# Kernel optimization log

Measured on AMD Instinct MI355X. Metric: run time of the kernel, lower is better.

The kernel has to match this reference:

```python
import jax, jax.numpy as jnp
import numpy as np

L, H, C, DH, FF = 6, 8, 512, 64, 2048
B, T, S = 64, 128, 128
EPS = 1e-5


def setup_inputs() -> dict:
    key = jax.random.key(0)
    ks = jax.random.split(key, 20)
    sc = 0.02
    def w(k, shape):
        return jax.random.normal(k, shape, dtype=jnp.float32) * sc
    inp = {
        "x": jax.random.normal(ks[0], (B, T, C), dtype=jnp.float32),
        "encoder_output": jax.random.normal(ks[1], (B, S, C), dtype=jnp.float32),
        # per-head self-attention projections, stacked over layers and heads
        "sa_wq": w(ks[2], (L, H, C, DH)), "sa_bq": w(ks[3], (L, H, DH)),
        "sa_wk": w(ks[4], (L, H, C, DH)), "sa_bk": w(ks[5], (L, H, DH)),
        "sa_wv": w(ks[6], (L, H, C, DH)), "sa_bv": w(ks[7], (L, H, DH)),
        # per-head cross-attention projections
        "ca_wq": w(ks[8], (L, H, C, DH)), "ca_bq": w(ks[9], (L, H, DH)),
        "ca_wk": w(ks[10], (L, H, C, DH)), "ca_bk": w(ks[11], (L, H, DH)),
        "ca_wv": w(ks[12], (L, H, C, DH)), "ca_bv": w(ks[13], (L, H, DH)),
        # feed-forward
        "ff_w1": w(ks[14], (L, C, FF)), "ff_b1": w(ks[15], (L, FF)),
        "ff_w2": w(ks[16], (L, FF, C)), "ff_b2": w(ks[17], (L, C)),
    }
    return inp


def _layer_norm_2d(x):
    # F.layer_norm(x, (T, C)): normalize jointly over last two dims, no affine
    mu = jnp.mean(x, axis=(1, 2), keepdims=True)
    var = jnp.var(x, axis=(1, 2), keepdims=True)
    return (x - mu) * jax.lax.rsqrt(var + EPS)


def _mha(qx, kvx, wq, bq, wk, bk, wv, bv):
    # wq/wk/wv: [H, C, DH]; per-head projections, vectorized over heads.
    q = jnp.einsum("btc,hcd->bhtd", qx, wq) + bq[:, None, :]
    k = jnp.einsum("bsc,hcd->bhsd", kvx, wk) + bk[:, None, :]
    v = jnp.einsum("bsc,hcd->bhsd", kvx, wv) + bv[:, None, :]
    scores = jax.nn.softmax(jnp.einsum("bhtd,bhsd->bhts", q, k) * (DH ** -0.5), axis=-1)
    out = jnp.einsum("bhts,bhsd->bhtd", scores, v)
    b, h, t, d = out.shape  # concat heads along feature dim
    return out.transpose(0, 2, 1, 3).reshape(b, t, h * d)


def reference(x, encoder_output, sa_wq, sa_bq, sa_wk, sa_bk, sa_wv, sa_bv,
              ca_wq, ca_bq, ca_wk, ca_bk, ca_wv, ca_bv,
              ff_w1, ff_b1, ff_w2, ff_b2):
    for l in range(L):
        # masked MHA (note: original code never applies the causal mask)
        x = x + _mha(x, x, sa_wq[l], sa_bq[l], sa_wk[l], sa_bk[l], sa_wv[l], sa_bv[l])
        x = _layer_norm_2d(x)
        # cross attention: q from decoder, k/v from encoder output
        x = x + _mha(x, encoder_output, ca_wq[l], ca_bq[l], ca_wk[l], ca_bk[l], ca_wv[l], ca_bv[l])
        x = _layer_norm_2d(x)
        # feed-forward
        h = jax.nn.relu(jnp.einsum("btc,cf->btf", x, ff_w1[l]) + ff_b1[l])
        x = x + (jnp.einsum("btf,fc->btc", h, ff_w2[l]) + ff_b2[l])
        x = _layer_norm_2d(x)
    return x
```

## Files before the change

kernel.cpp:

```cpp
#include <hip/hip_runtime.h>
#include <hip/hip_bf16.h>


typedef __bf16 bf16;
typedef bf16 bf16x8 __attribute__((ext_vector_type(8)));
typedef float f32x4 __attribute__((ext_vector_type(4)));

#define MFMA16(a, b, c) __builtin_amdgcn_mfma_f32_16x16x32_bf16(a, b, c, 0, 0, 0)

#define GLL16(gsrc, ldst)                                                          \
    __builtin_amdgcn_global_load_lds(                                              \
        (const __attribute__((address_space(1))) void*)(gsrc),                     \
        (__attribute__((address_space(3))) void*)(ldst), 16, 0, 0)

static constexpr int L_ = 6, C_ = 512, FF_ = 2048;
static constexpr int B_ = 64, T_ = 128;
static constexpr int M_ = B_ * T_;
static constexpr float LNINV = 1.f / 65536.f;
static constexpr float EPS_ = 1e-5f;

__global__ __launch_bounds__(256) void zero_all(
    float* __restrict__ csA, float* __restrict__ csQ, float* __restrict__ csF,
    float* __restrict__ part)
{
    const int i = blockIdx.x * 256 + threadIdx.x;
    if (i < 6 * 1536) csA[i] = 0.f;
    if (i < 6 * 512)  csQ[i] = 0.f;
    if (i < 6 * 2048) csF[i] = 0.f;
    if (i < 18 * 64 * 2) part[i] = 0.f;
}

__global__ __launch_bounds__(256) void init_x(
    const float* __restrict__ xin, float* __restrict__ y, bf16* __restrict__ yb)
{
    const size_t i = ((size_t)blockIdx.x * 256 + threadIdx.x) * 8;
    float4 f0 = *(const float4*)(xin + i);
    float4 f1 = *(const float4*)(xin + i + 4);
    *(float4*)(y + i) = f0;
    *(float4*)(y + i + 4) = f1;
    bf16x8 v = {(bf16)f0.x, (bf16)f0.y, (bf16)f0.z, (bf16)f0.w,
                (bf16)f1.x, (bf16)f1.y, (bf16)f1.z, (bf16)f1.w};
    *(bf16x8*)(yb + i) = v;
}

__global__ __launch_bounds__(256) void to_bf16(
    const float* __restrict__ in, bf16* __restrict__ out)
{
    const size_t i = ((size_t)blockIdx.x * 256 + threadIdx.x) * 8;
    float4 f0 = *(const float4*)(in + i);
    float4 f1 = *(const float4*)(in + i + 4);
    bf16x8 v = {(bf16)f0.x, (bf16)f0.y, (bf16)f0.z, (bf16)f0.w,
                (bf16)f1.x, (bf16)f1.y, (bf16)f1.z, (bf16)f1.w};
    *(bf16x8*)(out + i) = v;
}

__global__ __launch_bounds__(256) void ff_repack(
    const float* __restrict__ ff_w1, const float* __restrict__ ff_w2,
    bf16* __restrict__ W1, bf16* __restrict__ W2)
{
    __shared__ alignas(16) float t[64][68];
    const int z = blockIdx.z;
    const float* src;
    bf16* dst;
    int R, C, r0, c0;
    if (z < 6) {
        src = ff_w1 + (size_t)z * 512 * 2048;
        dst = W1 + (size_t)z * 2048 * 512;
        R = 512; C = 2048;
        r0 = blockIdx.y * 64;
        c0 = blockIdx.x * 64;
    } else {
        src = ff_w2 + (size_t)(z - 6) * 2048 * 512;
        dst = W2 + (size_t)(z - 6) * 512 * 2048;
        R = 2048; C = 512;
        r0 = (blockIdx.y * 4 + (blockIdx.x >> 3)) * 64;
        c0 = (blockIdx.x & 7) * 64;
    }
    const int tr = threadIdx.x >> 4;
    const int tc = (threadIdx.x & 15) * 4;
#pragma unroll
    for (int ro = 0; ro < 64; ro += 16)
        *(float4*)&t[tr + ro][tc] = *(const float4*)(src + (size_t)(r0 + tr + ro) * C + c0 + tc);
    __syncthreads();
    const int wc = (threadIdx.x & 7) * 8;
#pragma unroll
    for (int po = 0; po < 2; ++po) {
        const int oc = (threadIdx.x >> 3) + po * 32;
        bf16x8 v;
#pragma unroll
        for (int j = 0; j < 8; ++j) v[j] = (bf16)t[wc + j][oc];
        *(bf16x8*)(dst + (size_t)(c0 + oc) * R + r0 + wc) = v;
    }
}

__global__ __launch_bounds__(256) void head_repack(
    const float* __restrict__ sa_wq, const float* __restrict__ sa_wk,
    const float* __restrict__ sa_wv, const float* __restrict__ ca_wq,
    const float* __restrict__ ca_wk, const float* __restrict__ ca_wv,
    bf16* __restrict__ Wsa, bf16* __restrict__ Wcaq, bf16* __restrict__ Wcakv)
{
    __shared__ alignas(16) float t[64][68];
    const int z = blockIdx.z;
    const int type = z / 48, rem = z % 48, l = rem >> 3, h = rem & 7;
    const float* srcs[6] = {sa_wq, sa_wk, sa_wv, ca_wq, ca_wk, ca_wv};
    const float* s = srcs[type] + (size_t)(l * 8 + h) * 512 * 64;
    bf16* d;
    if (type < 3)       d = Wsa   + ((size_t)l * 1536 + type * 512 + h * 64) * 512;
    else if (type == 3) d = Wcaq  + ((size_t)l * 512 + h * 64) * 512;
    else                d = Wcakv + ((size_t)l * 1024 + (type - 4) * 512 + h * 64) * 512;
    const int r0 = blockIdx.y * 64;
    const int tr = threadIdx.x >> 4;
    const int tc = (threadIdx.x & 15) * 4;
#pragma unroll
    for (int ro = 0; ro < 64; ro += 16)
        *(float4*)&t[tr + ro][tc] = *(const float4*)(s + (size_t)(r0 + tr + ro) * 64 + tc);
    __syncthreads();
    const int wc = (threadIdx.x & 7) * 8;
#pragma unroll
    for (int po = 0; po < 2; ++po) {
        const int oc = (threadIdx.x >> 3) + po * 32;
        bf16x8 v;
#pragma unroll
        for (int j = 0; j < 8; ++j) v[j] = (bf16)t[wc + j][oc];
        *(bf16x8*)(d + (size_t)oc * 512 + r0 + wc) = v;
    }
}

__global__ __launch_bounds__(256) void colsum_all(
    const float* __restrict__ sa_wq, const float* __restrict__ sa_wk,
    const float* __restrict__ sa_wv, const float* __restrict__ ca_wq,
    const float* __restrict__ ff_w1,
    float* __restrict__ csA, float* __restrict__ csQ, float* __restrict__ csF)
{
    const int t = blockIdx.x * 256 + threadIdx.x;
    const int l = t >> 12, u = t & 4095;
    const int r0 = blockIdx.y * 64;
    const float* base;
    int stride;
    float* out;
    if (u < 1536) {
        const int p = u >> 9, h = (u >> 6) & 7, d = u & 63;
        const float* w = (p == 0) ? sa_wq : (p == 1) ? sa_wk : sa_wv;
        base = w + (size_t)(l * 8 + h) * 512 * 64 + d;
        stride = 64;
        out = &csA[l * 1536 + u];
    } else if (u < 2048) {
        const int v = u - 1536, h = v >> 6, d = v & 63;
        base = ca_wq + (size_t)(l * 8 + h) * 512 * 64 + d;
        stride = 64;
        out = &csQ[l * 512 + v];
    } else {
        const int f = u - 2048;
        base = ff_w1 + (size_t)l * 512 * 2048 + f;
        stride = 2048;
        out = &csF[l * 2048 + f];
    }
    const float* p = base + (size_t)r0 * stride;
    float s0 = 0.f, s1 = 0.f, s2 = 0.f, s3 = 0.f;
#pragma unroll 4
    for (int c = 0; c < 64; c += 4) {
        s0 += p[0];
        s1 += p[(size_t)stride];
        s2 += p[(size_t)2 * stride];
        s3 += p[(size_t)3 * stride];
        p += (size_t)4 * stride;
    }
    atomicAdd(out, (s0 + s1) + (s2 + s3));
}

template <int MODE, int BN>
__global__ __launch_bounds__(256, 4) void gemm_bt(
    const bf16* __restrict__ A, const bf16* __restrict__ BT,
    const float* __restrict__ b0, const float* __restrict__ b1,
    const float* __restrict__ b2, const float* __restrict__ cs,
    float2* __restrict__ part, int slotPrev, int slotNew,
    bf16* __restrict__ o0, bf16* __restrict__ o1, bf16* __restrict__ o2,
    float* __restrict__ y, bf16* __restrict__ ybf, int N, int K)
{
    constexpr int MI = 4;
    constexpr int NI = BN / 32;
    constexpr int BGLL = BN / 64;
    constexpr int VG = 2 + BGLL;
    __shared__ alignas(16) bf16 as[2][128][32];
    __shared__ alignas(16) bf16 bs[2][BN][32];
    const int tid = threadIdx.x, wave = tid >> 6, lane = tid & 63;

    const int gx = gridDim.x;
    int wgid = blockIdx.y * gx + blockIdx.x;
    {
        const int nwg = gx * gridDim.y;
        const int q = nwg >> 3, r = nwg & 7;
        const int xcd = wgid & 7, idx = wgid >> 3;
        wgid = (xcd < r ? xcd * (q + 1) : r * (q + 1) + (xcd - r) * q) + idx;
    }
    const int m0 = (wgid / gx) * 128, n0 = (wgid % gx) * BN;

    const int wr = (wave >> 1) * 64;
    const int wc = (wave & 1) * (BN / 2);
    const int fr = lane & 15, fq = lane >> 4;
    const int xr = fr & 3;

    float mu = 0.f, rstd = 1.f;
    if (slotPrev >= 0) {
        float2 p = part[slotPrev * 64 + (m0 >> 7)];
        mu = p.x * LNINV;
        rstd = rsqrtf(p.y * LNINV - mu * mu + EPS_);
    }

    const int rlane = lane >> 2;
    const int scol = ((lane & 3) ^ (rlane & 3)) * 8;
    const bf16* pa = A + (size_t)(m0 + wave * 32 + rlane) * K + scol;
    const bf16* pb = BT + (size_t)(n0 + wave * (BGLL * 16) + rlane) * K + scol;

    auto stage = [&](int buf, int k0) {
#pragma unroll
        for (int i = 0; i < 2; ++i)
            GLL16(pa + k0 + (size_t)(16 * i) * K, &as[buf][wave * 32 + 16 * i][0]);
#pragma unroll
        for (int i = 0; i < BGLL; ++i)
            GLL16(pb + k0 + (size_t)(16 * i) * K, &bs[buf][wave * (BGLL * 16) + 16 * i][0]);
    };

    f32x4 acc[MI][NI] = {};
    bf16x8 af[MI], bfv[NI];
    auto frags = [&](int buf) {
#pragma unroll
        for (int mi = 0; mi < MI; ++mi)
            af[mi] = *(const bf16x8*)&as[buf][wr + mi * 16 + fr][(fq ^ xr) << 3];
#pragma unroll
        for (int ni = 0; ni < NI; ++ni)
            bfv[ni] = *(const bf16x8*)&bs[buf][wc + ni * 16 + fr][(fq ^ xr) << 3];
    };
    auto cluster = [&]() {
#pragma unroll
        for (int mi = 0; mi < MI; ++mi)
#pragma unroll
            for (int ni = 0; ni < NI; ++ni)
                acc[mi][ni] = MFMA16(af[mi], bfv[ni], acc[mi][ni]);
    };

    const int nt = K >> 5;
    stage(0, 0);
    stage(1, 32);

    int cur = 0;
    for (int t = 0; t < nt - 1; ++t) {
        asm volatile("s_waitcnt vmcnt(%0)\n\ts_barrier" :: "n"(VG) : "memory");
        frags(cur);
        asm volatile("s_waitcnt lgkmcnt(0)\n\ts_barrier" ::: "memory");
        if (t + 2 < nt) stage(cur, (t + 2) << 5);
        cluster();
        cur ^= 1;
    }
    asm volatile("s_waitcnt vmcnt(0)\n\ts_barrier" ::: "memory");
    frags(cur);
    cluster();

    float s = 0.f, ss = 0.f;
    const float murs = mu * rstd;
#pragma unroll
    for (int mi = 0; mi < MI; ++mi) {
#pragma unroll
        for (int ni = 0; ni < NI; ++ni) {
            const int n = n0 + wc + ni * 16 + fr;
#pragma unroll
            for (int reg = 0; reg < 4; ++reg) {
                const int r = m0 + wr + mi * 16 + fq * 4 + reg;
                float val = acc[mi][ni][reg];
                if constexpr (MODE == 0) {
                    const int p = n >> 9, hd = n & 511, d = n & 63, hh = (n >> 6) & 7;
                    const int bb = r >> 7, tt = r & 127;
                    const float* bias = (p == 0) ? b0 : (p == 1 ? b1 : b2);
                    val = val * rstd + bias[hd] - murs * cs[n];
                    const size_t bh = (size_t)(bb * 8 + hh);
                    if (p == 0)      o0[(bh * 128 + tt) * 64 + d] = (bf16)val;
                    else if (p == 1) o1[(bh * 128 + tt) * 64 + d] = (bf16)val;
                    else             o2[(bh * 64 + d) * 128 + tt] = (bf16)val;
                } else if constexpr (MODE == 1) {
                    const int d = n & 63, hh = (n >> 6) & 7;
                    const int bb = r >> 7, tt = r & 127;
                    val = val * rstd + b0[n] - murs * cs[n];
                    o0[((size_t)(bb * 8 + hh) * 128 + tt) * 64 + d] = (bf16)val;
                } else if constexpr (MODE == 2) {
                    const int p = n >> 9, hd = n & 511, d = n & 63, hh = (n >> 6) & 7;
                    const int bb = r >> 7, tt = r & 127;
                    val += (p == 0) ? b1[hd] : b2[hd];
                    const size_t bh = (size_t)(bb * 8 + hh);
                    if (p == 0) o1[(bh * 128 + tt) * 64 + d] = (bf16)val;
                    else        o2[(bh * 64 + d) * 128 + tt] = (bf16)val;
                } else if constexpr (MODE == 3) {
                    val = val * rstd + b0[n] - murs * cs[n];
                    val = fmaxf(val, 0.f);
                    o0[(size_t)r * 2048 + n] = (bf16)val;
                } else {
                    const size_t idx = (size_t)r * 512 + n;
                    const float v = (y[idx] - mu) * rstd + val + b0[n];
                    y[idx] = v;
                    ybf[idx] = (bf16)v;
                    s += v;
                    ss += v * v;
                }
            }
        }
    }
    if constexpr (MODE == 4) {
        for (int off = 32; off; off >>= 1) { s += __shfl_xor(s, off); ss += __shfl_xor(ss, off); }
        __shared__ float rs[4], rss[4];
        if (lane == 0) { rs[wave] = s; rss[wave] = ss; }
        __syncthreads();
        if (tid == 0) {
            float2* dst = &part[slotNew * 64 + (m0 >> 7)];
            atomicAdd(&dst->x, rs[0] + rs[1] + rs[2] + rs[3]);
            atomicAdd(&dst->y, rss[0] + rss[1] + rss[2] + rss[3]);
        }
    }
}

__global__ __launch_bounds__(256) void attn_kernel(
    const bf16* __restrict__ q, const bf16* __restrict__ k,
    const bf16* __restrict__ vT, float* __restrict__ y, bf16* __restrict__ ybf,
    float2* __restrict__ part, int slotPrev, int slotNew)
{
    __shared__ alignas(16) bf16 sP[128][136];
    __shared__ float sPart[2][128];
    const int bh = blockIdx.x;
    const int bb = bh >> 3, hh = bh & 7;
    const bf16* Q = q + (size_t)bh * 128 * 64;
    const bf16* Kp = k + (size_t)bh * 128 * 64;
    const bf16* V = vT + (size_t)bh * 64 * 128;
    const int tid = threadIdx.x, wave = tid >> 6, lane = tid & 63;
    const int wr = (wave >> 1) * 64, wc = (wave & 1) * 64;
    const int fr = lane & 15, fq = lane >> 4;

    float mu = 0.f, rstd = 1.f;
    if (slotPrev >= 0) {
        float2 p = part[slotPrev * 64 + bb];
        mu = p.x * LNINV;
        rstd = rsqrtf(p.y * LNINV - mu * mu + EPS_);
    }

    f32x4 acc[4][4] = {};
#pragma unroll
    for (int k0 = 0; k0 < 64; k0 += 32) {
        bf16x8 af[4], bfv[4];
#pragma unroll
        for (int mi = 0; mi < 4; ++mi)
            af[mi] = *(const bf16x8*)(Q + (size_t)(wr + mi * 16 + fr) * 64 + k0 + fq * 8);
#pragma unroll
        for (int ni = 0; ni < 4; ++ni)
            bfv[ni] = *(const bf16x8*)(Kp + (size_t)(wc + ni * 16 + fr) * 64 + k0 + fq * 8);
#pragma unroll
        for (int mi = 0; mi < 4; ++mi)
#pragma unroll
            for (int ni = 0; ni < 4; ++ni)
                acc[mi][ni] = MFMA16(af[mi], bfv[ni], acc[mi][ni]);
    }

    const int colw = wave & 1;
#pragma unroll
    for (int mi = 0; mi < 4; ++mi) {
#pragma unroll
        for (int reg = 0; reg < 4; ++reg) {
            const int r = wr + mi * 16 + fq * 4 + reg;
            float rsum = 0.f;
#pragma unroll
            for (int ni = 0; ni < 4; ++ni) {
                const float e = __expf(acc[mi][ni][reg] * 0.125f);
                sP[r][wc + ni * 16 + fr] = (bf16)e;
                rsum += e;
            }
            rsum += __shfl_xor(rsum, 1);
            rsum += __shfl_xor(rsum, 2);
            rsum += __shfl_xor(rsum, 4);
            rsum += __shfl_xor(rsum, 8);
            if (fr == 0) sPart[colw][r] = rsum;
        }
    }
    __syncthreads();

    f32x4 acc2[2][4] = {};
#pragma unroll
    for (int k0 = 0; k0 < 128; k0 += 32) {
        bf16x8 af[2], bfv[4];
#pragma unroll
        for (int mi = 0; mi < 2; ++mi)
            af[mi] = *(const bf16x8*)&sP[wave * 32 + mi * 16 + fr][k0 + fq * 8];
#pragma unroll
        for (int ni = 0; ni < 4; ++ni)
            bfv[ni] = *(const bf16x8*)(V + (size_t)(ni * 16 + fr) * 128 + k0 + fq * 8);
#pragma unroll
        for (int mi = 0; mi < 2; ++mi)
#pragma unroll
            for (int ni = 0; ni < 4; ++ni)
                acc2[mi][ni] = MFMA16(af[mi], bfv[ni], acc2[mi][ni]);
    }

    float inv[2][4];
#pragma unroll
    for (int mi = 0; mi < 2; ++mi)
#pragma unroll
        for (int reg = 0; reg < 4; ++reg) {
            const int r = wave * 32 + mi * 16 + fq * 4 + reg;
            inv[mi][reg] = 1.f / (sPart[0][r] + sPart[1][r]);
        }

    float s = 0.f, ss = 0.f;
#pragma unroll
    for (int mi = 0; mi < 2; ++mi)
#pragma unroll
        for (int ni = 0; ni < 4; ++ni)
#pragma unroll
            for (int reg = 0; reg < 4; ++reg) {
                const int r = wave * 32 + mi * 16 + fq * 4 + reg;
                const int d = ni * 16 + fr;
                const size_t idx = ((size_t)(bb * 128 + r)) * 512 + hh * 64 + d;
                const float v = (y[idx] - mu) * rstd + acc2[mi][ni][reg] * inv[mi][reg];
                y[idx] = v;
                ybf[idx] = (bf16)v;
                s += v;
                ss += v * v;
            }
    for (int off = 32; off; off >>= 1) { s += __shfl_xor(s, off); ss += __shfl_xor(ss, off); }
    __shared__ float rs[4], rss[4];
    if (lane == 0) { rs[wave] = s; rss[wave] = ss; }
    __syncthreads();
    if (tid == 0) {
        float2* dst = &part[slotNew * 64 + bb];
        atomicAdd(&dst->x, rs[0] + rs[1] + rs[2] + rs[3]);
        atomicAdd(&dst->y, rss[0] + rss[1] + rss[2] + rss[3]);
    }
}

__global__ __launch_bounds__(256) void final_norm(
    const float* __restrict__ y, const float2* __restrict__ part, int slot,
    float* __restrict__ out)
{
    const size_t i = ((size_t)blockIdx.x * 256 + threadIdx.x) * 4;
    const int b = (int)(i >> 16);
    float2 p = part[slot * 64 + b];
    const float mu = p.x * LNINV;
    const float rstd = rsqrtf(p.y * LNINV - mu * mu + EPS_);
    float4 v = *(const float4*)(y + i);
    float4 o = {(v.x - mu) * rstd, (v.y - mu) * rstd, (v.z - mu) * rstd, (v.w - mu) * rstd};
    *(float4*)(out + i) = o;
}

extern "C" void kernel_launch(void* const* d_in, const int* in_sizes, int n_in,
                              void* d_out, int out_size, void* d_ws, size_t ws_size,
                              hipStream_t stream)
{
    (void)in_sizes; (void)n_in; (void)out_size; (void)ws_size;
    const float* x_in  = (const float*)d_in[0];
    const float* enc   = (const float*)d_in[1];
    const float* sa_wq = (const float*)d_in[2];
    const float* sa_bq = (const float*)d_in[3];
    const float* sa_wk = (const float*)d_in[4];
    const float* sa_bk = (const float*)d_in[5];
    const float* sa_wv = (const float*)d_in[6];
    const float* sa_bv = (const float*)d_in[7];
    const float* ca_wq = (const float*)d_in[8];
    const float* ca_bq = (const float*)d_in[9];
    const float* ca_wk = (const float*)d_in[10];
    const float* ca_bk = (const float*)d_in[11];
    const float* ca_wv = (const float*)d_in[12];
    const float* ca_bv = (const float*)d_in[13];
    const float* ff_w1 = (const float*)d_in[14];
    const float* ff_b1 = (const float*)d_in[15];
    const float* ff_w2 = (const float*)d_in[16];
    const float* ff_b2 = (const float*)d_in[17];

    char* wsp = (char*)d_ws;
    auto alloc = [&](size_t bytes) -> char* {
        char* p = wsp;
        wsp += (bytes + 255) & ~(size_t)255;
        return p;
    };
    float* y     = (float*)alloc((size_t)M_ * 512 * 4);
    bf16*  ybf   = (bf16*)alloc((size_t)M_ * 512 * 2);
    bf16*  encbf = (bf16*)alloc((size_t)M_ * 512 * 2);
    char*  shreg = alloc((size_t)M_ * 2048 * 2);
    bf16*  WsaA  = (bf16*)alloc((size_t)L_ * 1536 * 512 * 2);
    bf16*  WcaqA = (bf16*)alloc((size_t)L_ * 512 * 512 * 2);
    bf16*  WcakvA= (bf16*)alloc((size_t)L_ * 1024 * 512 * 2);
    bf16*  Wff1A = (bf16*)alloc((size_t)L_ * 2048 * 512 * 2);
    bf16*  Wff2A = (bf16*)alloc((size_t)L_ * 512 * 2048 * 2);
    float* csA   = (float*)alloc((size_t)L_ * 1536 * 4);
    float* csQ   = (float*)alloc((size_t)L_ * 512 * 4);
    float* csF   = (float*)alloc((size_t)L_ * 2048 * 4);
    float2* part = (float2*)alloc(18 * 64 * sizeof(float2));

    bf16* qb   = (bf16*)shreg;
    bf16* kb   = (bf16*)(shreg + (size_t)512 * 128 * 64 * 2);
    bf16* vTb  = (bf16*)(shreg + (size_t)2 * 512 * 128 * 64 * 2);
    bf16* hbuf = (bf16*)shreg;

    dim3 tb(256);
    zero_all<<<48, tb, 0, stream>>>(csA, csQ, csF, (float*)part);
    init_x<<<2048, tb, 0, stream>>>(x_in, y, ybf);
    to_bf16<<<2048, tb, 0, stream>>>(enc, encbf);
    head_repack<<<dim3(1, 8, 288), tb, 0, stream>>>(sa_wq, sa_wk, sa_wv, ca_wq, ca_wk, ca_wv,
                                                    WsaA, WcaqA, WcakvA);
    ff_repack<<<dim3(32, 8, 12), tb, 0, stream>>>(ff_w1, ff_w2, Wff1A, Wff2A);
    colsum_all<<<dim3(96, 8), tb, 0, stream>>>(sa_wq, sa_wk, sa_wv, ca_wq, ff_w1, csA, csQ, csF);

    for (int l = 0; l < L_; ++l) {
        const int sPrev = (l == 0) ? -1 : (l - 1) * 3 + 2;
        gemm_bt<0, 128><<<dim3(12, 64), tb, 0, stream>>>(ybf, WsaA + (size_t)l * 1536 * 512,
            sa_bq + l * 512, sa_bk + l * 512, sa_bv + l * 512, csA + l * 1536,
            part, sPrev, -1, qb, kb, vTb, nullptr, nullptr, 1536, 512);
        attn_kernel<<<512, tb, 0, stream>>>(qb, kb, vTb, y, ybf, part, sPrev, l * 3 + 0);
        gemm_bt<1, 64><<<dim3(8, 64), tb, 0, stream>>>(ybf, WcaqA + (size_t)l * 512 * 512,
            ca_bq + l * 512, nullptr, nullptr, csQ + l * 512,
            part, l * 3 + 0, -1, qb, nullptr, nullptr, nullptr, nullptr, 512, 512);
        gemm_bt<2, 128><<<dim3(8, 64), tb, 0, stream>>>(encbf, WcakvA + (size_t)l * 1024 * 512,
            nullptr, ca_bk + l * 512, ca_bv + l * 512, nullptr,
            part, -1, -1, nullptr, kb, vTb, nullptr, nullptr, 1024, 512);
        attn_kernel<<<512, tb, 0, stream>>>(qb, kb, vTb, y, ybf, part, l * 3 + 0, l * 3 + 1);
        gemm_bt<3, 128><<<dim3(16, 64), tb, 0, stream>>>(ybf, Wff1A + (size_t)l * 2048 * 512,
            ff_b1 + l * 2048, nullptr, nullptr, csF + l * 2048,
            part, l * 3 + 1, -1, hbuf, nullptr, nullptr, nullptr, nullptr, 2048, 512);
        gemm_bt<4, 64><<<dim3(8, 64), tb, 0, stream>>>(hbuf, Wff2A + (size_t)l * 512 * 2048,
            ff_b2 + l * 512, nullptr, nullptr, nullptr,
            part, l * 3 + 1, l * 3 + 2, nullptr, nullptr, nullptr, y, ybf, 512, 2048);
    }
    final_norm<<<4096, tb, 0, stream>>>(y, part, 17, (float*)d_out);
}
```

Baseline: 1.320 ms.

## Deepen GEMM LDS pipeline and fuse cross-attention Q and KV projections

The GEMM template gains a DEPTH parameter so global-to-LDS prefetch runs three or four stages ahead instead of two, hiding more load latency at the cost of extra LDS per block. The cross-attention Q projection (from the normalized decoder state) and the K/V projection (from the encoder) are merged into one launch of 12x64 blocks. Blocks choose their A operand and LayerNorm correction by column range. This removes one kernel launch per layer and fills the GPU with a single larger grid. The extra LDS may reduce occupancy.

```diff
diff --git a/kernel.cpp b/kernel.cpp
--- a/kernel.cpp
+++ b/kernel.cpp
@@ -97,7 +97,7 @@
     const float* __restrict__ sa_wq, const float* __restrict__ sa_wk,
     const float* __restrict__ sa_wv, const float* __restrict__ ca_wq,
     const float* __restrict__ ca_wk, const float* __restrict__ ca_wv,
-    bf16* __restrict__ Wsa, bf16* __restrict__ Wcaq, bf16* __restrict__ Wcakv)
+    bf16* __restrict__ Wsa, bf16* __restrict__ Wca)
 {
     __shared__ alignas(16) float t[64][68];
     const int z = blockIdx.z;
@@ -105,9 +105,8 @@
     const float* srcs[6] = {sa_wq, sa_wk, sa_wv, ca_wq, ca_wk, ca_wv};
     const float* s = srcs[type] + (size_t)(l * 8 + h) * 512 * 64;
     bf16* d;
-    if (type < 3)       d = Wsa   + ((size_t)l * 1536 + type * 512 + h * 64) * 512;
-    else if (type == 3) d = Wcaq  + ((size_t)l * 512 + h * 64) * 512;
-    else                d = Wcakv + ((size_t)l * 1024 + (type - 4) * 512 + h * 64) * 512;
+    if (type < 3) d = Wsa + ((size_t)l * 1536 + type * 512 + h * 64) * 512;
+    else          d = Wca + ((size_t)l * 1536 + (type - 3) * 512 + h * 64) * 512;
     const int r0 = blockIdx.y * 64;
     const int tr = threadIdx.x >> 4;
     const int tc = (threadIdx.x & 15) * 4;
@@ -168,7 +167,7 @@
     atomicAdd(out, (s0 + s1) + (s2 + s3));
 }
 
-template <int MODE, int BN>
+template <int MODE, int BN, int DEPTH>
 __global__ __launch_bounds__(256, 4) void gemm_bt(
     const bf16* __restrict__ A, const bf16* __restrict__ BT,
     const float* __restrict__ b0, const float* __restrict__ b1,
@@ -181,8 +180,8 @@
     constexpr int NI = BN / 32;
     constexpr int BGLL = BN / 64;
     constexpr int VG = 2 + BGLL;
-    __shared__ alignas(16) bf16 as[2][128][32];
-    __shared__ alignas(16) bf16 bs[2][BN][32];
+    __shared__ alignas(16) bf16 as[DEPTH][128][32];
+    __shared__ alignas(16) bf16 bs[DEPTH][BN][32];
     const int tid = threadIdx.x, wave = tid >> 6, lane = tid & 63;
 
     const int gx = gridDim.x;
@@ -200,8 +199,14 @@
     const int fr = lane & 15, fq = lane >> 4;
     const int xr = fr & 3;
 
+    const bf16* Abase = A;
+    bool fix = (slotPrev >= 0);
+    if constexpr (MODE == 5) {
+        if (n0 >= 512) { Abase = (const bf16*)ybf; fix = false; }
+    }
+
     float mu = 0.f, rstd = 1.f;
-    if (slotPrev >= 0) {
+    if (fix) {
         float2 p = part[slotPrev * 64 + (m0 >> 7)];
         mu = p.x * LNINV;
         rstd = rsqrtf(p.y * LNINV - mu * mu + EPS_);
@@ -209,7 +214,7 @@
 
     const int rlane = lane >> 2;
     const int scol = ((lane & 3) ^ (rlane & 3)) * 8;
-    const bf16* pa = A + (size_t)(m0 + wave * 32 + rlane) * K + scol;
+    const bf16* pa = Abase + (size_t)(m0 + wave * 32 + rlane) * K + scol;
     const bf16* pb = BT + (size_t)(n0 + wave * (BGLL * 16) + rlane) * K + scol;
 
     auto stage = [&](int buf, int k0) {
@@ -240,18 +245,35 @@
     };
 
     const int nt = K >> 5;
-    stage(0, 0);
-    stage(1, 32);
+#pragma unroll
+    for (int d = 0; d < DEPTH; ++d) stage(d, d << 5);
 
     int cur = 0;
-    for (int t = 0; t < nt - 1; ++t) {
-        asm volatile("s_waitcnt vmcnt(%0)\n\ts_barrier" :: "n"(VG) : "memory");
+    for (int t = 0; t < nt - DEPTH; ++t) {
+        asm volatile("s_waitcnt vmcnt(%0)\n\ts_barrier" :: "n"((DEPTH - 1) * VG) : "memory");
         frags(cur);
         asm volatile("s_waitcnt lgkmcnt(0)\n\ts_barrier" ::: "memory");
-        if (t + 2 < nt) stage(cur, (t + 2) << 5);
+        stage(cur, (t + DEPTH) << 5);
         cluster();
-        cur ^= 1;
-    }
+        cur = (cur + 1 == DEPTH) ? 0 : cur + 1;
+    }
+    if constexpr (DEPTH == 4) {
+        asm volatile("s_waitcnt vmcnt(%0)\n\ts_barrier" :: "n"(3 * VG) : "memory");
+        frags(cur);
+        asm volatile("s_waitcnt lgkmcnt(0)\n\ts_barrier" ::: "memory");
+        cluster();
+        cur = (cur + 1 == DEPTH) ? 0 : cur + 1;
+    }
+    asm volatile("s_waitcnt vmcnt(%0)\n\ts_barrier" :: "n"(2 * VG) : "memory");
+    frags(cur);
+    asm volatile("s_waitcnt lgkmcnt(0)\n\ts_barrier" ::: "memory");
+    cluster();
+    cur = (cur + 1 == DEPTH) ? 0 : cur + 1;
+    asm volatile("s_waitcnt vmcnt(%0)\n\ts_barrier" :: "n"(VG) : "memory");
+    frags(cur);
+    asm volatile("s_waitcnt lgkmcnt(0)\n\ts_barrier" ::: "memory");
+    cluster();
+    cur = (cur + 1 == DEPTH) ? 0 : cur + 1;
     asm volatile("s_waitcnt vmcnt(0)\n\ts_barrier" ::: "memory");
     frags(cur);
     cluster();
@@ -276,18 +298,20 @@
                     if (p == 0)      o0[(bh * 128 + tt) * 64 + d] = (bf16)val;
                     else if (p == 1) o1[(bh * 128 + tt) * 64 + d] = (bf16)val;
                     else             o2[(bh * 64 + d) * 128 + tt] = (bf16)val;
-                } else if constexpr (MODE == 1) {
-                    const int d = n & 63, hh = (n >> 6) & 7;
-                    const int bb = r >> 7, tt = r & 127;
-                    val = val * rstd + b0[n] - murs * cs[n];
-                    o0[((size_t)(bb * 8 + hh) * 128 + tt) * 64 + d] = (bf16)val;
-                } else if constexpr (MODE == 2) {
+                } else if constexpr (MODE == 5) {
                     const int p = n >> 9, hd = n & 511, d = n & 63, hh = (n >> 6) & 7;
                     const int bb = r >> 7, tt = r & 127;
-                    val += (p == 0) ? b1[hd] : b2[hd];
                     const size_t bh = (size_t)(bb * 8 + hh);
-                    if (p == 0) o1[(bh * 128 + tt) * 64 + d] = (bf16)val;
-                    else        o2[(bh * 64 + d) * 128 + tt] = (bf16)val;
+                    if (p == 0) {
+                        val = val * rstd + b0[n] - murs * cs[n];
+                        o0[(bh * 128 + tt) * 64 + d] = (bf16)val;
+                    } else if (p == 1) {
+                        val += b1[hd];
+                        o1[(bh * 128 + tt) * 64 + d] = (bf16)val;
+                    } else {
+                        val += b2[hd];
+                        o2[(bh * 64 + d) * 128 + tt] = (bf16)val;
+                    }
                 } else if constexpr (MODE == 3) {
                     val = val * rstd + b0[n] - murs * cs[n];
                     val = fmaxf(val, 0.f);
@@ -480,8 +504,7 @@
     bf16*  encbf = (bf16*)alloc((size_t)M_ * 512 * 2);
     char*  shreg = alloc((size_t)M_ * 2048 * 2);
     bf16*  WsaA  = (bf16*)alloc((size_t)L_ * 1536 * 512 * 2);
-    bf16*  WcaqA = (bf16*)alloc((size_t)L_ * 512 * 512 * 2);
-    bf16*  WcakvA= (bf16*)alloc((size_t)L_ * 1024 * 512 * 2);
+    bf16*  WcaA  = (bf16*)alloc((size_t)L_ * 1536 * 512 * 2);
     bf16*  Wff1A = (bf16*)alloc((size_t)L_ * 2048 * 512 * 2);
     bf16*  Wff2A = (bf16*)alloc((size_t)L_ * 512 * 2048 * 2);
     float* csA   = (float*)alloc((size_t)L_ * 1536 * 4);
@@ -499,27 +522,24 @@
     init_x<<<2048, tb, 0, stream>>>(x_in, y, ybf);
     to_bf16<<<2048, tb, 0, stream>>>(enc, encbf);
     head_repack<<<dim3(1, 8, 288), tb, 0, stream>>>(sa_wq, sa_wk, sa_wv, ca_wq, ca_wk, ca_wv,
-                                                    WsaA, WcaqA, WcakvA);
+                                                    WsaA, WcaA);
     ff_repack<<<dim3(32, 8, 12), tb, 0, stream>>>(ff_w1, ff_w2, Wff1A, Wff2A);
     colsum_all<<<dim3(96, 8), tb, 0, stream>>>(sa_wq, sa_wk, sa_wv, ca_wq, ff_w1, csA, csQ, csF);
 
     for (int l = 0; l < L_; ++l) {
         const int sPrev = (l == 0) ? -1 : (l - 1) * 3 + 2;
-        gemm_bt<0, 128><<<dim3(12, 64), tb, 0, stream>>>(ybf, WsaA + (size_t)l * 1536 * 512,
+        gemm_bt<0, 128, 3><<<dim3(12, 64), tb, 0, stream>>>(ybf, WsaA + (size_t)l * 1536 * 512,
             sa_bq + l * 512, sa_bk + l * 512, sa_bv + l * 512, csA + l * 1536,
             part, sPrev, -1, qb, kb, vTb, nullptr, nullptr, 1536, 512);
         attn_kernel<<<512, tb, 0, stream>>>(qb, kb, vTb, y, ybf, part, sPrev, l * 3 + 0);
-        gemm_bt<1, 64><<<dim3(8, 64), tb, 0, stream>>>(ybf, WcaqA + (size_t)l * 512 * 512,
-            ca_bq + l * 512, nullptr, nullptr, csQ + l * 512,
-            part, l * 3 + 0, -1, qb, nullptr, nullptr, nullptr, nullptr, 512, 512);
-        gemm_bt<2, 128><<<dim3(8, 64), tb, 0, stream>>>(encbf, WcakvA + (size_t)l * 1024 * 512,
-            nullptr, ca_bk + l * 512, ca_bv + l * 512, nullptr,
-            part, -1, -1, nullptr, kb, vTb, nullptr, nullptr, 1024, 512);
+        gemm_bt<5, 128, 3><<<dim3(12, 64), tb, 0, stream>>>(ybf, WcaA + (size_t)l * 1536 * 512,
+            ca_bq + l * 512, ca_bk + l * 512, ca_bv + l * 512, csQ + l * 512,
+            part, l * 3 + 0, -1, qb, kb, vTb, nullptr, encbf, 1536, 512);
         attn_kernel<<<512, tb, 0, stream>>>(qb, kb, vTb, y, ybf, part, l * 3 + 0, l * 3 + 1);
-        gemm_bt<3, 128><<<dim3(16, 64), tb, 0, stream>>>(ybf, Wff1A + (size_t)l * 2048 * 512,
+        gemm_bt<3, 128, 3><<<dim3(16, 64), tb, 0, stream>>>(ybf, Wff1A + (size_t)l * 2048 * 512,
             ff_b1 + l * 2048, nullptr, nullptr, csF + l * 2048,
             part, l * 3 + 1, -1, hbuf, nullptr, nullptr, nullptr, nullptr, 2048, 512);
-        gemm_bt<4, 64><<<dim3(8, 64), tb, 0, stream>>>(hbuf, Wff2A + (size_t)l * 512 * 2048,
+        gemm_bt<4, 64, 4><<<dim3(8, 64), tb, 0, stream>>>(hbuf, Wff2A + (size_t)l * 512 * 2048,
             ff_b2 + l * 512, nullptr, nullptr, nullptr,
             part, l * 3 + 1, l * 3 + 2, nullptr, nullptr, nullptr, y, ybf, 512, 2048);
     }
```

After: 1.348 ms. 2.1% more time.
